# Optimization experiments

Measured on AMD Instinct MI355X. Metric: run time of the kernel, lower is better.

Reference implementation:

```python
import jax, jax.numpy as jnp
import numpy as np

B, H, K, E = 8, 256, 256, 128
VOCAB, FVOCAB = 30000, 1000


def setup_inputs() -> dict:
    key = jax.random.key(0)
    k1, k2, k3, k4, k5, k6 = jax.random.split(key, 6)
    key_emb = jax.random.normal(k2, (VOCAB, E), dtype=jnp.float32)
    value_emb = jax.random.normal(k3, (FVOCAB, E), dtype=jnp.float32)
    # padding_idx=0 rows are zero
    key_emb = key_emb.at[0].set(0.0)
    value_emb = value_emb.at[0].set(0.0)
    return {
        "hidden": jax.random.normal(k1, (B, H, E), dtype=jnp.float32),
        "key_emb": key_emb,
        "value_emb": value_emb,
        "key_seq": jax.random.randint(k4, (B, K), 0, VOCAB, dtype=jnp.int64) if jax.config.jax_enable_x64 else jax.random.randint(k4, (B, K), 0, VOCAB).astype(jnp.int32),
        "value_seq": jax.random.randint(k5, (B, H, K), 0, FVOCAB).astype(jnp.int32),
        "mask_matrix": jax.random.randint(k6, (B, H, K), 0, 2).astype(jnp.int32),
    }


def reference(hidden, key_emb, value_emb, key_seq, value_seq, mask_matrix):
    scale = jnp.asarray(np.power(E, 0.5), dtype=jnp.float32)
    # embedding gathers (padding_idx=0 -> zero row, enforced in setup)
    k = key_emb[key_seq]            # [B, K, E]
    v = value_emb[value_seq]        # [B, H, K, E]
    # masked exp-normalize attention (manual, not softmax: no max-subtract)
    u = jnp.einsum('bhe,bke->bhk', hidden, k) / scale   # [B, H, K]
    delta = jnp.exp(u) * mask_matrix.astype(jnp.float32)
    p = delta / (jnp.sum(delta, axis=2, keepdims=True) + 1e-10)  # [B, H, K]
    # attention-weighted value aggregation
    o = jnp.einsum('bhk,bhke->bhe', p, v)               # [B, H, E]
    # nonzero-count averaging over H
    aspect_len = jnp.sum(o != 0, axis=1).astype(jnp.float32)     # [B, E]
    avg_o = jnp.sum(o, axis=1) / aspect_len                      # [B, E]
    return avg_o
```

## Files before the change

kernel.cpp:

```cpp
#include <hip/hip_runtime.h>
#include <math.h>

#define BB 8
#define HH 256
#define KK 256
#define EE 128

template <int CTRL, int RM>
__device__ __forceinline__ float dpp_add(float x) {
    int d = __builtin_amdgcn_update_dpp(0, __float_as_int(x), CTRL, RM, 0xf, true);
    return x + __int_as_float(d);
}
__device__ __forceinline__ float dpp_reduce_half(float x) {
    x = dpp_add<0x111, 0xf>(x);
    x = dpp_add<0x112, 0xf>(x);
    x = dpp_add<0x114, 0xf>(x);
    x = dpp_add<0x118, 0xf>(x);
    x = dpp_add<0x142, 0xa>(x);
    return x;
}
__device__ __forceinline__ float dpp_reduce_wave(float x) {
    x = dpp_reduce_half(x);
    x = dpp_add<0x143, 0xc>(x);
    return x;
}

__global__ __launch_bounds__(256) void kvmn_bh(
    const float* __restrict__ hidden,
    const float* __restrict__ key_emb,
    const float* __restrict__ value_emb,
    const int*   __restrict__ key_seq,
    const int*   __restrict__ value_seq,
    const int*   __restrict__ mask,
    float* __restrict__ o_ws)
{
    __shared__ float  sh_u[KK];
    __shared__ float  sh_part[4];
    __shared__ float4 sh_o4[8][32];

    const int bid  = blockIdx.x;
    const int b    = bid >> 8;
    const int h    = bid & 255;
    const int tid  = threadIdx.x;
    const int w    = tid >> 6;
    const int lane = tid & 63;
    const int half = lane >> 5;
    const int sub  = lane & 31;

    const int ksreg = key_seq[b * KK + tid];
    const int vsreg = value_seq[(size_t)(b * HH + h) * KK + tid];
    const int my_mask = mask[(size_t)(b * HH + h) * KK + tid];

    const float4 h4 = *(const float4*)&hidden[(size_t)(b * HH + h) * EE + sub * 4];

    const float inv_scale = 0.08838834764831845f;

    #pragma unroll 16
    for (int i = 0; i < 32; ++i) {
        const int    row = __shfl(ksreg, half * 32 + i, 64);
        const float4 kv  = *(const float4*)&key_emb[(size_t)row * EE + sub * 4];
        float part = kv.x * h4.x + kv.y * h4.y + kv.z * h4.z + kv.w * h4.w;
        part = dpp_reduce_half(part);
        if (sub == 31) sh_u[w * 64 + half * 32 + i] = part * inv_scale;
    }
    __syncthreads();

    const float d = expf(sh_u[tid]) * (float)my_mask;
    float s = dpp_reduce_wave(d);
    if (lane == 63) sh_part[w] = s;
    __syncthreads();
    const float denom = sh_part[0] + sh_part[1] + sh_part[2] + sh_part[3];
    const float pk = d * (1.0f / (denom + 1e-10f));

    float4 acc = make_float4(0.f, 0.f, 0.f, 0.f);
    #pragma unroll 16
    for (int i = 0; i < 32; ++i) {
        const int    src = half * 32 + i;
        const float  p   = __shfl(pk, src, 64);
        const int    row = __shfl(vsreg, src, 64);
        const float4 v   = *(const float4*)&value_emb[(size_t)row * EE + sub * 4];
        acc.x += p * v.x;
        acc.y += p * v.y;
        acc.z += p * v.z;
        acc.w += p * v.w;
    }
    sh_o4[w * 2 + half][sub] = acc;
    __syncthreads();

    if (tid < 32) {
        float4 t = sh_o4[0][tid];
        #pragma unroll
        for (int r = 1; r < 8; ++r) {
            const float4 q = sh_o4[r][tid];
            t.x += q.x; t.y += q.y; t.z += q.z; t.w += q.w;
        }
        *(float4*)&o_ws[(size_t)(b * HH + h) * EE + tid * 4] = t;
    }
}

__global__ __launch_bounds__(256) void kvmn_reduce(
    const float* __restrict__ o_ws,
    float* __restrict__ out)
{
    __shared__ float sh_sum[256];
    __shared__ int   sh_cnt[256];

    const int b  = blockIdx.x;
    const int t  = threadIdx.x;
    const int e  = t & 127;
    const int hh = t >> 7;

    float sum = 0.0f;
    int   cnt = 0;
    const float* base = o_ws + (size_t)(b * HH + hh * 128) * EE + e;
    #pragma unroll 8
    for (int h = 0; h < 128; ++h) {
        const float v = base[(size_t)h * EE];
        sum += v;
        cnt += (v != 0.0f) ? 1 : 0;
    }
    sh_sum[t] = sum;
    sh_cnt[t] = cnt;
    __syncthreads();
    if (t < 128) {
        const float s = sh_sum[t] + sh_sum[t + 128];
        const int   c = sh_cnt[t] + sh_cnt[t + 128];
        out[b * EE + t] = s / (float)c;
    }
}

extern "C" void kernel_launch(void* const* d_in, const int* in_sizes, int n_in,
                              void* d_out, int out_size, void* d_ws, size_t ws_size,
                              hipStream_t stream) {
    const float* hidden    = (const float*)d_in[0];
    const float* key_emb   = (const float*)d_in[1];
    const float* value_emb = (const float*)d_in[2];
    const int*   key_seq   = (const int*)d_in[3];
    const int*   value_seq = (const int*)d_in[4];
    const int*   mask      = (const int*)d_in[5];

    float* o_ws = (float*)d_ws;

    kvmn_bh<<<BB * HH, 256, 0, stream>>>(hidden, key_emb, value_emb,
                                         key_seq, value_seq, mask, o_ws);
    kvmn_reduce<<<BB, 256, 0, stream>>>(o_ws, (float*)d_out);
    (void)in_sizes; (void)n_in; (void)out_size; (void)ws_size;
}
```

Measured before the change: 102.7 us.

## Process four heads per block to reuse gathered key embeddings

Each block now handles four consecutive h rows for one batch instead of one. Every gathered key_emb row is reused across four hidden vectors, cutting key gathers and the grid size by four. Attention weights and premultiplied value row offsets are staged in shared memory instead of being broadcast with per-iteration shuffles. The cost is more registers and shared memory per block and only 512 blocks, which may lower occupancy and latency hiding for the value gathers.

```diff
diff --git a/kernel.cpp b/kernel.cpp
--- a/kernel.cpp
+++ b/kernel.cpp
@@ -5,6 +5,7 @@
 #define HH 256
 #define KK 256
 #define EE 128
+#define GG 4
 
 template <int CTRL, int RM>
 __device__ __forceinline__ float dpp_add(float x) {
@@ -25,7 +26,7 @@
     return x;
 }
 
-__global__ __launch_bounds__(256) void kvmn_bh(
+__global__ __launch_bounds__(256) void kvmn_bh4(
     const float* __restrict__ hidden,
     const float* __restrict__ key_emb,
     const float* __restrict__ value_emb,
@@ -34,13 +35,14 @@
     const int*   __restrict__ mask,
     float* __restrict__ o_ws)
 {
-    __shared__ float  sh_u[KK];
-    __shared__ float  sh_part[4];
-    __shared__ float4 sh_o4[8][32];
+    __shared__ float  sh_u[GG][KK];
+    __shared__ float  sh_part[GG][4];
+    __shared__ float2 sh_pv[GG][KK];
+    __shared__ float4 sh_o4[GG][8][32];
 
     const int bid  = blockIdx.x;
-    const int b    = bid >> 8;
-    const int h    = bid & 255;
+    const int b    = bid >> 6;
+    const int h0   = (bid & 63) << 2;
     const int tid  = threadIdx.x;
     const int w    = tid >> 6;
     const int lane = tid & 63;
@@ -48,53 +50,87 @@
     const int sub  = lane & 31;
 
     const int ksreg = key_seq[b * KK + tid];
-    const int vsreg = value_seq[(size_t)(b * HH + h) * KK + tid];
-    const int my_mask = mask[(size_t)(b * HH + h) * KK + tid];
+    int vs[GG], mk[GG];
+    #pragma unroll
+    for (int g = 0; g < GG; ++g) {
+        vs[g] = value_seq[(size_t)(b * HH + h0 + g) * KK + tid];
+        mk[g] = mask[(size_t)(b * HH + h0 + g) * KK + tid];
+    }
 
-    const float4 h4 = *(const float4*)&hidden[(size_t)(b * HH + h) * EE + sub * 4];
+    float4 hq0 = *(const float4*)&hidden[(size_t)(b * HH + h0 + 0) * EE + sub * 4];
+    float4 hq1 = *(const float4*)&hidden[(size_t)(b * HH + h0 + 1) * EE + sub * 4];
+    float4 hq2 = *(const float4*)&hidden[(size_t)(b * HH + h0 + 2) * EE + sub * 4];
+    float4 hq3 = *(const float4*)&hidden[(size_t)(b * HH + h0 + 3) * EE + sub * 4];
 
     const float inv_scale = 0.08838834764831845f;
 
-    #pragma unroll 16
+    #pragma unroll 8
     for (int i = 0; i < 32; ++i) {
+        const int    k   = w * 64 + half * 32 + i;
         const int    row = __shfl(ksreg, half * 32 + i, 64);
         const float4 kv  = *(const float4*)&key_emb[(size_t)row * EE + sub * 4];
-        float part = kv.x * h4.x + kv.y * h4.y + kv.z * h4.z + kv.w * h4.w;
-        part = dpp_reduce_half(part);
-        if (sub == 31) sh_u[w * 64 + half * 32 + i] = part * inv_scale;
+        float p0 = kv.x * hq0.x + kv.y * hq0.y + kv.z * hq0.z + kv.w * hq0.w;
+        float p1 = kv.x * hq1.x + kv.y * hq1.y + kv.z * hq1.z + kv.w * hq1.w;
+        float p2 = kv.x * hq2.x + kv.y * hq2.y + kv.z * hq2.z + kv.w * hq2.w;
+        float p3 = kv.x * hq3.x + kv.y * hq3.y + kv.z * hq3.z + kv.w * hq3.w;
+        p0 = dpp_reduce_half(p0) * inv_scale;
+        p1 = dpp_reduce_half(p1) * inv_scale;
+        p2 = dpp_reduce_half(p2) * inv_scale;
+        p3 = dpp_reduce_half(p3) * inv_scale;
+        if (sub == 31) {
+            sh_u[0][k] = p0;
+            sh_u[1][k] = p1;
+            sh_u[2][k] = p2;
+            sh_u[3][k] = p3;
+        }
     }
     __syncthreads();
 
-    const float d = expf(sh_u[tid]) * (float)my_mask;
-    float s = dpp_reduce_wave(d);
-    if (lane == 63) sh_part[w] = s;
+    float dreg[GG];
+    #pragma unroll
+    for (int g = 0; g < GG; ++g) {
+        dreg[g] = expf(sh_u[g][tid]) * (float)mk[g];
+        const float s = dpp_reduce_wave(dreg[g]);
+        if (lane == 63) sh_part[g][w] = s;
+    }
     __syncthreads();
-    const float denom = sh_part[0] + sh_part[1] + sh_part[2] + sh_part[3];
-    const float pk = d * (1.0f / (denom + 1e-10f));
-
-    float4 acc = make_float4(0.f, 0.f, 0.f, 0.f);
-    #pragma unroll 16
-    for (int i = 0; i < 32; ++i) {
-        const int    src = half * 32 + i;
-        const float  p   = __shfl(pk, src, 64);
-        const int    row = __shfl(vsreg, src, 64);
-        const float4 v   = *(const float4*)&value_emb[(size_t)row * EE + sub * 4];
-        acc.x += p * v.x;
-        acc.y += p * v.y;
-        acc.z += p * v.z;
-        acc.w += p * v.w;
+    #pragma unroll
+    for (int g = 0; g < GG; ++g) {
+        const float denom = sh_part[g][0] + sh_part[g][1] + sh_part[g][2] + sh_part[g][3];
+        const float pk    = dreg[g] * (1.0f / (denom + 1e-10f));
+        sh_pv[g][tid] = make_float2(pk, __int_as_float(vs[g] << 7));
     }
-    sh_o4[w * 2 + half][sub] = acc;
     __syncthreads();
 
-    if (tid < 32) {
-        float4 t = sh_o4[0][tid];
+    const int kbase = w * 64 + half * 32;
+    #pragma unroll
+    for (int g = 0; g < GG; ++g) {
+        float4 acc = make_float4(0.f, 0.f, 0.f, 0.f);
+        #pragma unroll 8
+        for (int i = 0; i < 32; ++i) {
+            const float2 pv = sh_pv[g][kbase + i];
+            const float  p  = pv.x;
+            const int    ro = __float_as_int(pv.y);
+            const float4 v  = *(const float4*)&value_emb[(size_t)ro + sub * 4];
+            acc.x += p * v.x;
+            acc.y += p * v.y;
+            acc.z += p * v.z;
+            acc.w += p * v.w;
+        }
+        sh_o4[g][w * 2 + half][sub] = acc;
+    }
+    __syncthreads();
+
+    if (tid < 128) {
+        const int g   = tid >> 5;
+        const int col = tid & 31;
+        float4 t = sh_o4[g][0][col];
         #pragma unroll
         for (int r = 1; r < 8; ++r) {
-            const float4 q = sh_o4[r][tid];
+            const float4 q = sh_o4[g][r][col];
             t.x += q.x; t.y += q.y; t.z += q.z; t.w += q.w;
         }
-        *(float4*)&o_ws[(size_t)(b * HH + h) * EE + tid * 4] = t;
+        *(float4*)&o_ws[(size_t)(b * HH + h0 + g) * EE + col * 4] = t;
     }
 }
 
@@ -141,8 +177,8 @@
 
     float* o_ws = (float*)d_ws;
 
-    kvmn_bh<<<BB * HH, 256, 0, stream>>>(hidden, key_emb, value_emb,
-                                         key_seq, value_seq, mask, o_ws);
+    kvmn_bh4<<<BB * (HH / GG), 256, 0, stream>>>(hidden, key_emb, value_emb,
+                                                 key_seq, value_seq, mask, o_ws);
     kvmn_reduce<<<BB, 256, 0, stream>>>(o_ws, (float*)d_out);
     (void)in_sizes; (void)n_in; (void)out_size; (void)ws_size;
 }
```

Result: no change. 103.5 us (+0.8%).
